# Kernel optimization log

Measured on AMD Instinct MI355X. Metric: run time of the kernel, lower is better.

## Reference

```python
import jax, jax.numpy as jnp
import numpy as np

D_MODEL = 768
HIDDEN = 2048  # round(768*8/3)=2048, already a multiple of 64
N_EXPERTS = 8
ALPHA = 0.05  # load_balance_alpha


def setup_inputs() -> dict:
    key = jax.random.key(0)
    k0, k1, k2, k3, k4 = jax.random.split(key, 5)
    x = jax.random.normal(k0, (2, 2048, D_MODEL), dtype=jnp.float32)
    wg_w = jax.random.normal(k1, (N_EXPERTS, D_MODEL), dtype=jnp.float32) * 0.02
    wg_b = jnp.zeros((N_EXPERTS,), dtype=jnp.float32)
    Wu = jax.random.normal(k2, (N_EXPERTS, D_MODEL, HIDDEN), dtype=jnp.float32) * 0.02
    Wv = jax.random.normal(k3, (N_EXPERTS, D_MODEL, HIDDEN), dtype=jnp.float32) * 0.02
    Wd = jax.random.normal(k4, (N_EXPERTS, HIDDEN, D_MODEL), dtype=jnp.float32) * 0.02
    return {"x": x, "wg_w": wg_w, "wg_b": wg_b, "Wu": Wu, "Wv": Wv, "Wd": Wd}


def reference(x, wg_w, wg_b, Wu, Wv, Wd):
    b, t, d = x.shape
    xf = x.reshape(b * t, d)  # [N, d]

    # ---- Top1Router (eval mode: temp=1, no noise, z_loss_coef=0) ----
    logits = xf @ wg_w.T + wg_b            # [N, E]
    probs = jax.nn.softmax(logits, axis=-1)
    top1_idx = jnp.argmax(logits, axis=-1)  # [N]
    top1_p = jnp.take_along_axis(probs, top1_idx[:, None], axis=1)[:, 0]  # [N]

    # aux loss: me and ce computed under no_grad in the torch source -> stop_gradient
    one_hot = jax.nn.one_hot(top1_idx, N_EXPERTS, dtype=probs.dtype)
    me = jax.lax.stop_gradient(one_hot.mean(axis=0))   # [E]
    ce = jax.lax.stop_gradient(probs.mean(axis=0))     # [E]
    aux = ALPHA * N_EXPERTS * jnp.sum(me * ce)

    # ---- Dropless dispatch: per-expert masked SwiGLU, combined with top1 gate ----
    gate = top1_p[:, None]  # [N, 1]
    y = jnp.zeros_like(xf)
    for e in range(N_EXPERTS):
        mask = (top1_idx == e)[:, None]            # [N, 1]
        xe = jnp.where(mask, xf, 0.0)              # zero-out non-routed tokens (no biases -> exact)
        u = xe @ Wu[e]                              # [N, H]
        v = xe @ Wv[e]                              # [N, H]
        ye = (jax.nn.silu(u) * v) @ Wd[e]           # [N, d]
        y = y + jnp.where(mask, ye * gate, 0.0)
    return y.reshape(b, t, d), aux
```

## Files before the change

kernel.cpp:

```cpp
#include <hip/hip_runtime.h>
#include <cstdint>
#include <cstddef>

#define TOK 4096
#define DM 768
#define HID 2048
#define NE 8

typedef __attribute__((ext_vector_type(8))) short bf16x8;
typedef __attribute__((ext_vector_type(4))) float f32x4;

#define ASYNC16(GP, LP) \
  __builtin_amdgcn_global_load_lds((__attribute__((address_space(1))) void*)(GP), \
                                   (__attribute__((address_space(3))) void*)(LP), 16, 0, 0)

__device__ __forceinline__ unsigned short f2bf(float f) {
  unsigned int u = __float_as_uint(f);
  u += 0x7FFF + ((u >> 16) & 1);
  return (unsigned short)(u >> 16);
}
__device__ __forceinline__ unsigned int pack2(float a, float b) {
  return (unsigned)f2bf(a) | ((unsigned)f2bf(b) << 16);
}
__device__ __forceinline__ int padded_off(const int* counts, int e) {
  int o = 0;
  for (int i = 0; i < e; ++i) o += (counts[i] + 127) & ~127;
  return o;
}

__global__ __launch_bounds__(256)
void k_gate(const float* __restrict__ x, const float* __restrict__ wgw,
            const float* __restrict__ wgb,
            int* __restrict__ eidx, float* __restrict__ gatep,
            float* __restrict__ cepart)
{
  __shared__ float ce_loc[4][NE];
  const int lane = threadIdx.x & 63;
  const int w = threadIdx.x >> 6;
  const int t = blockIdx.x * 4 + w;
  float acc[NE];
#pragma unroll
  for (int e = 0; e < NE; ++e) acc[e] = 0.f;
  const float* xr = x + (size_t)t * DM;
#pragma unroll
  for (int j = 0; j < DM / 64; ++j) {
    float xv = xr[j * 64 + lane];
#pragma unroll
    for (int e = 0; e < NE; ++e) acc[e] += xv * wgw[e * DM + j * 64 + lane];
  }
#pragma unroll
  for (int e = 0; e < NE; ++e) {
    float v = acc[e];
#pragma unroll
    for (int off = 32; off >= 1; off >>= 1) v += __shfl_xor(v, off);
    acc[e] = v + wgb[e];
  }
  float mx = acc[0]; int ai = 0;
#pragma unroll
  for (int e = 1; e < NE; ++e) if (acc[e] > mx) { mx = acc[e]; ai = e; }
  float p[NE]; float se = 0.f;
#pragma unroll
  for (int e = 0; e < NE; ++e) { p[e] = expf(acc[e] - mx); se += p[e]; }
  float inv = 1.f / se;
  if (lane == 0) {
#pragma unroll
    for (int e = 0; e < NE; ++e) ce_loc[w][e] = p[e] * inv;
    eidx[t] = ai;
    gatep[t] = p[ai] * inv;
  }
  __syncthreads();
  if (threadIdx.x < NE) {
    float s = ce_loc[0][threadIdx.x] + ce_loc[1][threadIdx.x]
            + ce_loc[2][threadIdx.x] + ce_loc[3][threadIdx.x];
    cepart[blockIdx.x * NE + threadIdx.x] = s;
  }
}

__global__ __launch_bounds__(256)
void k_count(const int* __restrict__ eidx, const float* __restrict__ gatep,
             const float* __restrict__ cepart,
             int* __restrict__ prow_arr, int* __restrict__ tlist,
             float* __restrict__ gate_b, int* __restrict__ counts_g,
             float* __restrict__ aux_out)
{
  __shared__ int hist[256][NE];
  __shared__ float fs[256][NE];
  __shared__ int po_s[NE], cnt_s[NE];
  const int tid = threadIdx.x;
  int own[NE], v[NE], el[16];
#pragma unroll
  for (int e = 0; e < NE; ++e) own[e] = 0;
#pragma unroll
  for (int j = 0; j < 16; ++j) {
    el[j] = eidx[tid * 16 + j];
#pragma unroll
    for (int e = 0; e < NE; ++e) own[e] += (el[j] == e) ? 1 : 0;
  }
#pragma unroll
  for (int e = 0; e < NE; ++e) { v[e] = own[e]; hist[tid][e] = v[e]; }
  __syncthreads();
  for (int st = 1; st < 256; st <<= 1) {
    int add[NE];
#pragma unroll
    for (int e = 0; e < NE; ++e) add[e] = (tid >= st) ? hist[tid - st][e] : 0;
    __syncthreads();
#pragma unroll
    for (int e = 0; e < NE; ++e) { v[e] += add[e]; hist[tid][e] = v[e]; }
    __syncthreads();
  }
  if (tid == 0) {
    int o = 0;
#pragma unroll
    for (int e = 0; e < NE; ++e) {
      int c = hist[255][e];
      cnt_s[e] = c; counts_g[e] = c; po_s[e] = o;
      o += (c + 127) & ~127;
    }
  }
  __syncthreads();
  int run[NE];
#pragma unroll
  for (int e = 0; e < NE; ++e) run[e] = po_s[e] + v[e] - own[e];
#pragma unroll
  for (int j = 0; j < 16; ++j) {
    const int t = tid * 16 + j;
    const int e = el[j];
    int p = 0;
#pragma unroll
    for (int k = 0; k < NE; ++k) if (e == k) p = run[k]++;
    prow_arr[t] = p;
    tlist[p] = t;
    gate_b[p] = gatep[t];
  }
  float s[NE];
#pragma unroll
  for (int e = 0; e < NE; ++e) s[e] = 0.f;
  for (int bb = tid; bb < 1024; bb += 256)
#pragma unroll
    for (int e = 0; e < NE; ++e) s[e] += cepart[bb * NE + e];
#pragma unroll
  for (int e = 0; e < NE; ++e) fs[tid][e] = s[e];
  __syncthreads();
  for (int st = 128; st > 0; st >>= 1) {
    if (tid < st)
#pragma unroll
      for (int e = 0; e < NE; ++e) fs[tid][e] += fs[tid + st][e];
    __syncthreads();
  }
  if (tid == 0) {
    float aux = 0.f;
    for (int e = 0; e < NE; ++e)
      aux += ((float)cnt_s[e] / 4096.f) * (fs[0][e] / 4096.f);
    aux_out[0] = 0.05f * 8.f * aux;
  }
}

__global__ __launch_bounds__(256)
void k2_scatter_zero(const float* __restrict__ x, const int* __restrict__ prow_arr,
                     unsigned short* __restrict__ xb, float* __restrict__ y)
{
  const int b = blockIdx.x;
  if (b < 1024) {
    const int lane = threadIdx.x & 63;
    const int w = threadIdx.x >> 6;
    const int t = b * 4 + w;
    const int prow = prow_arr[t];
    const float4* src4 = (const float4*)(x + (size_t)t * DM);
    uint2* dst = (uint2*)(xb + (size_t)prow * DM);
#pragma unroll
    for (int c = 0; c < 3; ++c) {
      float4 v = src4[lane + c * 64];
      uint2 d; d.x = pack2(v.x, v.y); d.y = pack2(v.z, v.w);
      dst[lane + c * 64] = d;
    }
  } else {
    float4* y4 = (float4*)y;
    const int base = (b - 1024) * 1536 + threadIdx.x;
#pragma unroll
    for (int c = 0; c < 6; ++c) {
      float4 z; z.x = 0.f; z.y = 0.f; z.z = 0.f; z.w = 0.f;
      y4[base + c * 256] = z;
    }
  }
}

__device__ __forceinline__ bool tile_lookup(const int* __restrict__ counts,
                                            int tile, int& e, int& tm) {
  int acc = 0, fe = -1, ftm = 0;
#pragma unroll
  for (int i = 0; i < NE; ++i) {
    int nt = (counts[i] + 255) >> 8;
    if (fe < 0 && tile < acc + nt) { fe = i; ftm = tile - acc; }
    acc += nt;
  }
  if (fe < 0) return false;
  e = fe; tm = ftm;
  return true;
}

__global__ __launch_bounds__(512, 2)
void k_ffn1(const float* __restrict__ Wu, const float* __restrict__ Wv,
            const unsigned short* __restrict__ xb, const float* __restrict__ gate_b,
            const int* __restrict__ counts, unsigned short* __restrict__ h)
{
  const int bid = blockIdx.x;
  const int tn = bid & 15;
  const int tile = bid >> 4;
  int e, tm;
  if (!tile_lookup(counts, tile, e, tm)) return;
  const int Me = counts[e];
  const int prowbase = padded_off(counts, e) + tm * 256;

  __shared__ __align__(16) char Sh[65536];

  const int tid = threadIdx.x;
  const int lane = tid & 63;
  const int w = tid >> 6;
  const int wm = w >> 1, wn = w & 1;

  const int c0 = w * 2, c1 = w * 2 + 1;
  const int mA0 = c0 * 16 + (lane >> 2), sA0 = lane & 3;
  const int ko0 = (sA0 - mA0 - (mA0 >> 2)) & 3;
  const char* aSrc0 = (const char*)xb + (size_t)(prowbase + mA0) * (DM * 2) + ko0 * 16;
  const int mA1 = c1 * 16 + (lane >> 2), sA1 = lane & 3;
  const int ko1 = (sA1 - mA1 - (mA1 >> 2)) & 3;
  const char* aSrc1 = (const char*)xb + (size_t)(prowbase + mA1) * (DM * 2) + ko1 * 16;

  const int koW = w & 3;
  const int nloc = (w >> 2) * 64 + lane;
  const unsigned offBw = (unsigned)(nloc * 4 + ((koW + nloc + (nloc >> 2)) & 3)) * 16;
  const int ncol = tn * 128 + nloc;
  const float* srcU = Wu + (size_t)e * DM * HID + (size_t)(koW * 8) * HID + ncol;
  const float* srcV = Wv + (size_t)e * DM * HID + (size_t)(koW * 8) * HID + ncol;

  const int lc = lane & 15, q = lane >> 4;
  unsigned offA[4], offU[4], offV[4];
#pragma unroll
  for (int i = 0; i < 4; ++i) {
    int m = wm * 64 + i * 16 + lc;
    offA[i] = (unsigned)(m * 4 + ((q + m + (m >> 2)) & 3)) * 16;
    int n = wn * 64 + i * 16 + lc;
    unsigned ob = (unsigned)(n * 4 + ((q + n + (n >> 2)) & 3)) * 16;
    offU[i] = 16384u + ob;
    offV[i] = 24576u + ob;
  }

  f32x4 accU[4][4], accV[4][4];
#pragma unroll
  for (int i = 0; i < 4; ++i)
#pragma unroll
    for (int j = 0; j < 4; ++j)
#pragma unroll
      for (int k = 0; k < 4; ++k) { accU[i][j][k] = 0.f; accV[i][j][k] = 0.f; }

  float fu[8], fv[8];
  ASYNC16(aSrc0, Sh + c0 * 1024); aSrc0 += 64;
  ASYNC16(aSrc1, Sh + c1 * 1024); aSrc1 += 64;
#pragma unroll
  for (int j = 0; j < 8; ++j) { fu[j] = srcU[(size_t)j * HID]; fv[j] = srcV[(size_t)j * HID]; }
  srcU += (size_t)32 * HID; srcV += (size_t)32 * HID;
  {
    uint4 up, vp;
    up.x = pack2(fu[0], fu[1]); up.y = pack2(fu[2], fu[3]);
    up.z = pack2(fu[4], fu[5]); up.w = pack2(fu[6], fu[7]);
    vp.x = pack2(fv[0], fv[1]); vp.y = pack2(fv[2], fv[3]);
    vp.z = pack2(fv[4], fv[5]); vp.w = pack2(fv[6], fv[7]);
    *(uint4*)(Sh + 16384 + offBw) = up;
    *(uint4*)(Sh + 24576 + offBw) = vp;
  }
  __syncthreads();

  for (int kt = 0; kt < 24; ++kt) {
    char* bufc = Sh + (unsigned)(kt & 1) * 32768u;
    char* bufn = Sh + (unsigned)((kt + 1) & 1) * 32768u;
    const bool more = (kt + 1) < 24;
    if (more) {
      ASYNC16(aSrc0, bufn + c0 * 1024); aSrc0 += 64;
      ASYNC16(aSrc1, bufn + c1 * 1024); aSrc1 += 64;
#pragma unroll
      for (int j = 0; j < 8; ++j) { fu[j] = srcU[(size_t)j * HID]; fv[j] = srcV[(size_t)j * HID]; }
      srcU += (size_t)32 * HID; srcV += (size_t)32 * HID;
    }
    bf16x8 a[4], bu[4], bv[4];
#pragma unroll
    for (int i = 0; i < 4; ++i) a[i] = *(const bf16x8*)(bufc + offA[i]);
#pragma unroll
    for (int j = 0; j < 4; ++j) {
      bu[j] = *(const bf16x8*)(bufc + offU[j]);
      bv[j] = *(const bf16x8*)(bufc + offV[j]);
    }
#pragma unroll
    for (int i = 0; i < 4; ++i)
#pragma unroll
      for (int j = 0; j < 4; ++j) {
        accU[i][j] = __builtin_amdgcn_mfma_f32_16x16x32_bf16(a[i], bu[j], accU[i][j], 0, 0, 0);
        accV[i][j] = __builtin_amdgcn_mfma_f32_16x16x32_bf16(a[i], bv[j], accV[i][j], 0, 0, 0);
      }
    if (more) {
      uint4 up, vp;
      up.x = pack2(fu[0], fu[1]); up.y = pack2(fu[2], fu[3]);
      up.z = pack2(fu[4], fu[5]); up.w = pack2(fu[6], fu[7]);
      vp.x = pack2(fv[0], fv[1]); vp.y = pack2(fv[2], fv[3]);
      vp.z = pack2(fv[4], fv[5]); vp.w = pack2(fv[6], fv[7]);
      *(uint4*)(bufn + 16384 + offBw) = up;
      *(uint4*)(bufn + 24576 + offBw) = vp;
    }
    __syncthreads();
  }

  const int colbase = tn * 128 + wn * 64;
  const int rlane = (lane >> 4) * 4;
  const int clane = lane & 15;
#pragma unroll
  for (int i = 0; i < 4; ++i) {
#pragma unroll
    for (int rr = 0; rr < 4; ++rr) {
      int rowIn = wm * 64 + i * 16 + rlane + rr;
      if (tm * 256 + rowIn < Me) {
        int prow = prowbase + rowIn;
        float g = gate_b[prow];
        unsigned short* hp = h + (size_t)prow * HID + colbase + clane;
#pragma unroll
        for (int j = 0; j < 4; ++j) {
          float u_ = accU[i][j][rr];
          float v_ = accV[i][j][rr];
          float sv = u_ / (1.f + expf(-u_));
          hp[j * 16] = f2bf(sv * v_ * g);
        }
      }
    }
  }
}

__global__ __launch_bounds__(512, 2)
void k_ffn2(const float* __restrict__ Wd, const unsigned short* __restrict__ h,
            const int* __restrict__ counts, const int* __restrict__ tlist,
            float* __restrict__ y)
{
  const int bid = blockIdx.x;
  const int inner = bid % 24;
  const int tn = inner % 6;
  const int sk = inner / 6;
  const int tile = bid / 24;
  int e, tm;
  if (!tile_lookup(counts, tile, e, tm)) return;
  const int Me = counts[e];
  const int prowbase = padded_off(counts, e) + tm * 256;

  __shared__ __align__(16) char Sh[49152];

  const int tid = threadIdx.x;
  const int lane = tid & 63;
  const int w = tid >> 6;
  const int wm = w >> 1, wn = w & 1;

  const int c0 = w * 2, c1 = w * 2 + 1;
  const int mA0 = c0 * 16 + (lane >> 2), sA0 = lane & 3;
  const int ko0 = (sA0 - mA0 - (mA0 >> 2)) & 3;
  const char* aSrc0 = (const char*)h + (size_t)(prowbase + mA0) * (HID * 2) + sk * 1024 + ko0 * 16;
  const int mA1 = c1 * 16 + (lane >> 2), sA1 = lane & 3;
  const int ko1 = (sA1 - mA1 - (mA1 >> 2)) & 3;
  const char* aSrc1 = (const char*)h + (size_t)(prowbase + mA1) * (HID * 2) + sk * 1024 + ko1 * 16;

  const int nloc = tid & 127;
  const int koW = tid >> 7;
  const unsigned offBw = (unsigned)(nloc * 4 + ((koW + nloc + (nloc >> 2)) & 3)) * 16;
  const int ncol = tn * 128 + nloc;
  const float* srcD = Wd + (size_t)e * HID * DM + (size_t)(sk * 512 + koW * 8) * DM + ncol;

  const int lc = lane & 15, q = lane >> 4;
  unsigned offA[4], offBr[4];
#pragma unroll
  for (int i = 0; i < 4; ++i) {
    int m = wm * 64 + i * 16 + lc;
    offA[i] = (unsigned)(m * 4 + ((q + m + (m >> 2)) & 3)) * 16;
    int n = wn * 64 + i * 16 + lc;
    offBr[i] = 16384u + (unsigned)(n * 4 + ((q + n + (n >> 2)) & 3)) * 16;
  }

  f32x4 acc[4][4];
#pragma unroll
  for (int i = 0; i < 4; ++i)
#pragma unroll
    for (int j = 0; j < 4; ++j)
#pragma unroll
      for (int k = 0; k < 4; ++k) acc[i][j][k] = 0.f;

  float fd[8];
  ASYNC16(aSrc0, Sh + c0 * 1024); aSrc0 += 64;
  ASYNC16(aSrc1, Sh + c1 * 1024); aSrc1 += 64;
#pragma unroll
  for (int j = 0; j < 8; ++j) fd[j] = srcD[(size_t)j * DM];
  srcD += (size_t)32 * DM;
  {
    uint4 dp;
    dp.x = pack2(fd[0], fd[1]); dp.y = pack2(fd[2], fd[3]);
    dp.z = pack2(fd[4], fd[5]); dp.w = pack2(fd[6], fd[7]);
    *(uint4*)(Sh + 16384 + offBw) = dp;
  }
  __syncthreads();

  for (int kt = 0; kt < 16; ++kt) {
    char* bufc = Sh + (unsigned)(kt & 1) * 24576u;
    char* bufn = Sh + (unsigned)((kt + 1) & 1) * 24576u;
    const bool more = (kt + 1) < 16;
    if (more) {
      ASYNC16(aSrc0, bufn + c0 * 1024); aSrc0 += 64;
      ASYNC16(aSrc1, bufn + c1 * 1024); aSrc1 += 64;
#pragma unroll
      for (int j = 0; j < 8; ++j) fd[j] = srcD[(size_t)j * DM];
      srcD += (size_t)32 * DM;
    }
    bf16x8 a[4], b[4];
#pragma unroll
    for (int i = 0; i < 4; ++i) a[i] = *(const bf16x8*)(bufc + offA[i]);
#pragma unroll
    for (int j = 0; j < 4; ++j) b[j] = *(const bf16x8*)(bufc + offBr[j]);
#pragma unroll
    for (int i = 0; i < 4; ++i)
#pragma unroll
      for (int j = 0; j < 4; ++j)
        acc[i][j] = __builtin_amdgcn_mfma_f32_16x16x32_bf16(a[i], b[j], acc[i][j], 0, 0, 0);
    if (more) {
      uint4 dp;
      dp.x = pack2(fd[0], fd[1]); dp.y = pack2(fd[2], fd[3]);
      dp.z = pack2(fd[4], fd[5]); dp.w = pack2(fd[6], fd[7]);
      *(uint4*)(bufn + 16384 + offBw) = dp;
    }
    __syncthreads();
  }

  const int colbase = tn * 128 + wn * 64;
  const int rlane = (lane >> 4) * 4;
  const int clane = lane & 15;
#pragma unroll
  for (int i = 0; i < 4; ++i) {
#pragma unroll
    for (int rr = 0; rr < 4; ++rr) {
      int rowIn = wm * 64 + i * 16 + rlane + rr;
      if (tm * 256 + rowIn < Me) {
        int tok = tlist[prowbase + rowIn];
        float* yp = y + (size_t)tok * DM + colbase + clane;
#pragma unroll
        for (int j = 0; j < 4; ++j) atomicAdd(&yp[j * 16], acc[i][j][rr]);
      }
    }
  }
}

extern "C" void kernel_launch(void* const* d_in, const int* in_sizes, int n_in,
                              void* d_out, int out_size, void* d_ws, size_t ws_size,
                              hipStream_t stream)
{
  const float* x   = (const float*)d_in[0];
  const float* wgw = (const float*)d_in[1];
  const float* wgb = (const float*)d_in[2];
  const float* Wu  = (const float*)d_in[3];
  const float* Wv  = (const float*)d_in[4];
  const float* Wd  = (const float*)d_in[5];
  float* out = (float*)d_out;

  char* ws = (char*)d_ws;
  int*   counts = (int*)(ws + 0);
  int*   eidx   = (int*)(ws + 256);
  float* gatep  = (float*)(ws + 16640);
  int*   prow   = (int*)(ws + 33024);
  float* cepart = (float*)(ws + 49408);
  int*   tlist  = (int*)(ws + 82176);
  float* gate_b = (float*)(ws + 102656);
  unsigned short* xb  = (unsigned short*)(ws + 123136);
  unsigned short* h   = (unsigned short*)(ws + 7987456);

  k_gate<<<1024, 256, 0, stream>>>(x, wgw, wgb, eidx, gatep, cepart);
  k_count<<<1, 256, 0, stream>>>(eidx, gatep, cepart, prow, tlist, gate_b,
                                 counts, out + (size_t)TOK * DM);
  k2_scatter_zero<<<1536, 256, 0, stream>>>(x, prow, xb, out);
  k_ffn1<<<24 * 16, 512, 0, stream>>>(Wu, Wv, xb, gate_b, counts, h);
  k_ffn2<<<24 * 24, 512, 0, stream>>>(Wd, h, counts, tlist, out);
}
```

Baseline: 347.8 us.

## Halve FFN row tiles to 128 tokens with 256-thread blocks and float2 weight loads

Both expert FFN kernels now use 128-row token tiles instead of 256, with 4-wave blocks instead of 8 and smaller double-buffered LDS. Tile lookup and the launch grids change to match (up to 40 tiles per expert dimension). The weight staging is remapped so each thread loads two adjacent fp32 columns with float2 loads and writes two bf16 LDS rows. The aim is more blocks and higher occupancy, with less padding waste on partially filled expert tiles. The cost is that each expert's fp32 weight slice is re-read by roughly twice as many tiles, which raises global/L2 weight traffic.

```diff
diff --git a/kernel.cpp b/kernel.cpp
--- a/kernel.cpp
+++ b/kernel.cpp
@@ -189,7 +189,7 @@
   int acc = 0, fe = -1, ftm = 0;
 #pragma unroll
   for (int i = 0; i < NE; ++i) {
-    int nt = (counts[i] + 255) >> 8;
+    int nt = (counts[i] + 127) >> 7;
     if (fe < 0 && tile < acc + nt) { fe = i; ftm = tile - acc; }
     acc += nt;
   }
@@ -198,7 +198,7 @@
   return true;
 }
 
-__global__ __launch_bounds__(512, 2)
+__global__ __launch_bounds__(256, 3)
 void k_ffn1(const float* __restrict__ Wu, const float* __restrict__ Wv,
             const unsigned short* __restrict__ xb, const float* __restrict__ gate_b,
             const int* __restrict__ counts, unsigned short* __restrict__ h)
@@ -209,16 +209,16 @@
   int e, tm;
   if (!tile_lookup(counts, tile, e, tm)) return;
   const int Me = counts[e];
-  const int prowbase = padded_off(counts, e) + tm * 256;
-
-  __shared__ __align__(16) char Sh[65536];
+  const int prowbase = padded_off(counts, e) + tm * 128;
+
+  __shared__ __align__(16) char Sh[49152];
 
   const int tid = threadIdx.x;
   const int lane = tid & 63;
   const int w = tid >> 6;
   const int wm = w >> 1, wn = w & 1;
 
-  const int c0 = w * 2, c1 = w * 2 + 1;
+  const int c0 = w * 2, c1 = c0 + 1;
   const int mA0 = c0 * 16 + (lane >> 2), sA0 = lane & 3;
   const int ko0 = (sA0 - mA0 - (mA0 >> 2)) & 3;
   const char* aSrc0 = (const char*)xb + (size_t)(prowbase + mA0) * (DM * 2) + ko0 * 16;
@@ -226,12 +226,12 @@
   const int ko1 = (sA1 - mA1 - (mA1 >> 2)) & 3;
   const char* aSrc1 = (const char*)xb + (size_t)(prowbase + mA1) * (DM * 2) + ko1 * 16;
 
-  const int koW = w & 3;
-  const int nloc = (w >> 2) * 64 + lane;
-  const unsigned offBw = (unsigned)(nloc * 4 + ((koW + nloc + (nloc >> 2)) & 3)) * 16;
-  const int ncol = tn * 128 + nloc;
-  const float* srcU = Wu + (size_t)e * DM * HID + (size_t)(koW * 8) * HID + ncol;
-  const float* srcV = Wv + (size_t)e * DM * HID + (size_t)(koW * 8) * HID + ncol;
+  const int koW = w;
+  const int n0 = lane * 2, n1 = n0 + 1;
+  const unsigned offB0 = (unsigned)(n0 * 4 + ((koW + n0 + (n0 >> 2)) & 3)) * 16;
+  const unsigned offB1 = (unsigned)(n1 * 4 + ((koW + n1 + (n1 >> 2)) & 3)) * 16;
+  const float* srcU = Wu + (size_t)e * DM * HID + (size_t)(koW * 8) * HID + tn * 128 + n0;
+  const float* srcV = Wv + (size_t)e * DM * HID + (size_t)(koW * 8) * HID + tn * 128 + n0;
 
   const int lc = lane & 15, q = lane >> 4;
   unsigned offA[4], offU[4], offV[4];
@@ -241,8 +241,8 @@
     offA[i] = (unsigned)(m * 4 + ((q + m + (m >> 2)) & 3)) * 16;
     int n = wn * 64 + i * 16 + lc;
     unsigned ob = (unsigned)(n * 4 + ((q + n + (n >> 2)) & 3)) * 16;
-    offU[i] = 16384u + ob;
-    offV[i] = 24576u + ob;
+    offU[i] = 8192u + ob;
+    offV[i] = 16384u + ob;
   }
 
   f32x4 accU[4][4], accV[4][4];
@@ -253,32 +253,44 @@
 #pragma unroll
       for (int k = 0; k < 4; ++k) { accU[i][j][k] = 0.f; accV[i][j][k] = 0.f; }
 
-  float fu[8], fv[8];
+  float2 fu[8], fv[8];
   ASYNC16(aSrc0, Sh + c0 * 1024); aSrc0 += 64;
   ASYNC16(aSrc1, Sh + c1 * 1024); aSrc1 += 64;
 #pragma unroll
-  for (int j = 0; j < 8; ++j) { fu[j] = srcU[(size_t)j * HID]; fv[j] = srcV[(size_t)j * HID]; }
+  for (int j = 0; j < 8; ++j) {
+    fu[j] = *(const float2*)(srcU + (size_t)j * HID);
+    fv[j] = *(const float2*)(srcV + (size_t)j * HID);
+  }
   srcU += (size_t)32 * HID; srcV += (size_t)32 * HID;
   {
-    uint4 up, vp;
-    up.x = pack2(fu[0], fu[1]); up.y = pack2(fu[2], fu[3]);
-    up.z = pack2(fu[4], fu[5]); up.w = pack2(fu[6], fu[7]);
-    vp.x = pack2(fv[0], fv[1]); vp.y = pack2(fv[2], fv[3]);
-    vp.z = pack2(fv[4], fv[5]); vp.w = pack2(fv[6], fv[7]);
-    *(uint4*)(Sh + 16384 + offBw) = up;
-    *(uint4*)(Sh + 24576 + offBw) = vp;
+    uint4 u0, u1, v0, v1;
+    u0.x = pack2(fu[0].x, fu[1].x); u0.y = pack2(fu[2].x, fu[3].x);
+    u0.z = pack2(fu[4].x, fu[5].x); u0.w = pack2(fu[6].x, fu[7].x);
+    u1.x = pack2(fu[0].y, fu[1].y); u1.y = pack2(fu[2].y, fu[3].y);
+    u1.z = pack2(fu[4].y, fu[5].y); u1.w = pack2(fu[6].y, fu[7].y);
+    v0.x = pack2(fv[0].x, fv[1].x); v0.y = pack2(fv[2].x, fv[3].x);
+    v0.z = pack2(fv[4].x, fv[5].x); v0.w = pack2(fv[6].x, fv[7].x);
+    v1.x = pack2(fv[0].y, fv[1].y); v1.y = pack2(fv[2].y, fv[3].y);
+    v1.z = pack2(fv[4].y, fv[5].y); v1.w = pack2(fv[6].y, fv[7].y);
+    *(uint4*)(Sh + 8192 + offB0) = u0;
+    *(uint4*)(Sh + 8192 + offB1) = u1;
+    *(uint4*)(Sh + 16384 + offB0) = v0;
+    *(uint4*)(Sh + 16384 + offB1) = v1;
   }
   __syncthreads();
 
   for (int kt = 0; kt < 24; ++kt) {
-    char* bufc = Sh + (unsigned)(kt & 1) * 32768u;
-    char* bufn = Sh + (unsigned)((kt + 1) & 1) * 32768u;
+    char* bufc = Sh + (unsigned)(kt & 1) * 24576u;
+    char* bufn = Sh + (unsigned)((kt + 1) & 1) * 24576u;
     const bool more = (kt + 1) < 24;
     if (more) {
       ASYNC16(aSrc0, bufn + c0 * 1024); aSrc0 += 64;
       ASYNC16(aSrc1, bufn + c1 * 1024); aSrc1 += 64;
 #pragma unroll
-      for (int j = 0; j < 8; ++j) { fu[j] = srcU[(size_t)j * HID]; fv[j] = srcV[(size_t)j * HID]; }
+      for (int j = 0; j < 8; ++j) {
+        fu[j] = *(const float2*)(srcU + (size_t)j * HID);
+        fv[j] = *(const float2*)(srcV + (size_t)j * HID);
+      }
       srcU += (size_t)32 * HID; srcV += (size_t)32 * HID;
     }
     bf16x8 a[4], bu[4], bv[4];
@@ -297,13 +309,19 @@
         accV[i][j] = __builtin_amdgcn_mfma_f32_16x16x32_bf16(a[i], bv[j], accV[i][j], 0, 0, 0);
       }
     if (more) {
-      uint4 up, vp;
-      up.x = pack2(fu[0], fu[1]); up.y = pack2(fu[2], fu[3]);
-      up.z = pack2(fu[4], fu[5]); up.w = pack2(fu[6], fu[7]);
-      vp.x = pack2(fv[0], fv[1]); vp.y = pack2(fv[2], fv[3]);
-      vp.z = pack2(fv[4], fv[5]); vp.w = pack2(fv[6], fv[7]);
-      *(uint4*)(bufn + 16384 + offBw) = up;
-      *(uint4*)(bufn + 24576 + offBw) = vp;
+      uint4 u0, u1, v0, v1;
+      u0.x = pack2(fu[0].x, fu[1].x); u0.y = pack2(fu[2].x, fu[3].x);
+      u0.z = pack2(fu[4].x, fu[5].x); u0.w = pack2(fu[6].x, fu[7].x);
+      u1.x = pack2(fu[0].y, fu[1].y); u1.y = pack2(fu[2].y, fu[3].y);
+      u1.z = pack2(fu[4].y, fu[5].y); u1.w = pack2(fu[6].y, fu[7].y);
+      v0.x = pack2(fv[0].x, fv[1].x); v0.y = pack2(fv[2].x, fv[3].x);
+      v0.z = pack2(fv[4].x, fv[5].x); v0.w = pack2(fv[6].x, fv[7].x);
+      v1.x = pack2(fv[0].y, fv[1].y); v1.y = pack2(fv[2].y, fv[3].y);
+      v1.z = pack2(fv[4].y, fv[5].y); v1.w = pack2(fv[6].y, fv[7].y);
+      *(uint4*)(bufn + 8192 + offB0) = u0;
+      *(uint4*)(bufn + 8192 + offB1) = u1;
+      *(uint4*)(bufn + 16384 + offB0) = v0;
+      *(uint4*)(bufn + 16384 + offB1) = v1;
     }
     __syncthreads();
   }
@@ -316,7 +334,7 @@
 #pragma unroll
     for (int rr = 0; rr < 4; ++rr) {
       int rowIn = wm * 64 + i * 16 + rlane + rr;
-      if (tm * 256 + rowIn < Me) {
+      if (tm * 128 + rowIn < Me) {
         int prow = prowbase + rowIn;
         float g = gate_b[prow];
         unsigned short* hp = h + (size_t)prow * HID + colbase + clane;
@@ -332,7 +350,7 @@
   }
 }
 
-__global__ __launch_bounds__(512, 2)
+__global__ __launch_bounds__(256, 4)
 void k_ffn2(const float* __restrict__ Wd, const unsigned short* __restrict__ h,
             const int* __restrict__ counts, const int* __restrict__ tlist,
             float* __restrict__ y)
@@ -345,16 +363,16 @@
   int e, tm;
   if (!tile_lookup(counts, tile, e, tm)) return;
   const int Me = counts[e];
-  const int prowbase = padded_off(counts, e) + tm * 256;
-
-  __shared__ __align__(16) char Sh[49152];
+  const int prowbase = padded_off(counts, e) + tm * 128;
+
+  __shared__ __align__(16) char Sh[32768];
 
   const int tid = threadIdx.x;
   const int lane = tid & 63;
   const int w = tid >> 6;
   const int wm = w >> 1, wn = w & 1;
 
-  const int c0 = w * 2, c1 = w * 2 + 1;
+  const int c0 = w * 2, c1 = c0 + 1;
   const int mA0 = c0 * 16 + (lane >> 2), sA0 = lane & 3;
   const int ko0 = (sA0 - mA0 - (mA0 >> 2)) & 3;
   const char* aSrc0 = (const char*)h + (size_t)(prowbase + mA0) * (HID * 2) + sk * 1024 + ko0 * 16;
@@ -362,11 +380,11 @@
   const int ko1 = (sA1 - mA1 - (mA1 >> 2)) & 3;
   const char* aSrc1 = (const char*)h + (size_t)(prowbase + mA1) * (HID * 2) + sk * 1024 + ko1 * 16;
 
-  const int nloc = tid & 127;
-  const int koW = tid >> 7;
-  const unsigned offBw = (unsigned)(nloc * 4 + ((koW + nloc + (nloc >> 2)) & 3)) * 16;
-  const int ncol = tn * 128 + nloc;
-  const float* srcD = Wd + (size_t)e * HID * DM + (size_t)(sk * 512 + koW * 8) * DM + ncol;
+  const int koW = w;
+  const int n0 = lane * 2, n1 = n0 + 1;
+  const unsigned offB0 = (unsigned)(n0 * 4 + ((koW + n0 + (n0 >> 2)) & 3)) * 16;
+  const unsigned offB1 = (unsigned)(n1 * 4 + ((koW + n1 + (n1 >> 2)) & 3)) * 16;
+  const float* srcD = Wd + (size_t)e * HID * DM + (size_t)(sk * 512 + koW * 8) * DM + tn * 128 + n0;
 
   const int lc = lane & 15, q = lane >> 4;
   unsigned offA[4], offBr[4];
@@ -375,7 +393,7 @@
     int m = wm * 64 + i * 16 + lc;
     offA[i] = (unsigned)(m * 4 + ((q + m + (m >> 2)) & 3)) * 16;
     int n = wn * 64 + i * 16 + lc;
-    offBr[i] = 16384u + (unsigned)(n * 4 + ((q + n + (n >> 2)) & 3)) * 16;
+    offBr[i] = 8192u + (unsigned)(n * 4 + ((q + n + (n >> 2)) & 3)) * 16;
   }
 
   f32x4 acc[4][4];
@@ -386,29 +404,32 @@
 #pragma unroll
       for (int k = 0; k < 4; ++k) acc[i][j][k] = 0.f;
 
-  float fd[8];
+  float2 fd[8];
   ASYNC16(aSrc0, Sh + c0 * 1024); aSrc0 += 64;
   ASYNC16(aSrc1, Sh + c1 * 1024); aSrc1 += 64;
 #pragma unroll
-  for (int j = 0; j < 8; ++j) fd[j] = srcD[(size_t)j * DM];
+  for (int j = 0; j < 8; ++j) fd[j] = *(const float2*)(srcD + (size_t)j * DM);
   srcD += (size_t)32 * DM;
   {
-    uint4 dp;
-    dp.x = pack2(fd[0], fd[1]); dp.y = pack2(fd[2], fd[3]);
-    dp.z = pack2(fd[4], fd[5]); dp.w = pack2(fd[6], fd[7]);
-    *(uint4*)(Sh + 16384 + offBw) = dp;
+    uint4 d0, d1;
+    d0.x = pack2(fd[0].x, fd[1].x); d0.y = pack2(fd[2].x, fd[3].x);
+    d0.z = pack2(fd[4].x, fd[5].x); d0.w = pack2(fd[6].x, fd[7].x);
+    d1.x = pack2(fd[0].y, fd[1].y); d1.y = pack2(fd[2].y, fd[3].y);
+    d1.z = pack2(fd[4].y, fd[5].y); d1.w = pack2(fd[6].y, fd[7].y);
+    *(uint4*)(Sh + 8192 + offB0) = d0;
+    *(uint4*)(Sh + 8192 + offB1) = d1;
   }
   __syncthreads();
 
   for (int kt = 0; kt < 16; ++kt) {
-    char* bufc = Sh + (unsigned)(kt & 1) * 24576u;
-    char* bufn = Sh + (unsigned)((kt + 1) & 1) * 24576u;
+    char* bufc = Sh + (unsigned)(kt & 1) * 16384u;
+    char* bufn = Sh + (unsigned)((kt + 1) & 1) * 16384u;
     const bool more = (kt + 1) < 16;
     if (more) {
       ASYNC16(aSrc0, bufn + c0 * 1024); aSrc0 += 64;
       ASYNC16(aSrc1, bufn + c1 * 1024); aSrc1 += 64;
 #pragma unroll
-      for (int j = 0; j < 8; ++j) fd[j] = srcD[(size_t)j * DM];
+      for (int j = 0; j < 8; ++j) fd[j] = *(const float2*)(srcD + (size_t)j * DM);
       srcD += (size_t)32 * DM;
     }
     bf16x8 a[4], b[4];
@@ -422,10 +443,13 @@
       for (int j = 0; j < 4; ++j)
         acc[i][j] = __builtin_amdgcn_mfma_f32_16x16x32_bf16(a[i], b[j], acc[i][j], 0, 0, 0);
     if (more) {
-      uint4 dp;
-      dp.x = pack2(fd[0], fd[1]); dp.y = pack2(fd[2], fd[3]);
-      dp.z = pack2(fd[4], fd[5]); dp.w = pack2(fd[6], fd[7]);
-      *(uint4*)(bufn + 16384 + offBw) = dp;
+      uint4 d0, d1;
+      d0.x = pack2(fd[0].x, fd[1].x); d0.y = pack2(fd[2].x, fd[3].x);
+      d0.z = pack2(fd[4].x, fd[5].x); d0.w = pack2(fd[6].x, fd[7].x);
+      d1.x = pack2(fd[0].y, fd[1].y); d1.y = pack2(fd[2].y, fd[3].y);
+      d1.z = pack2(fd[4].y, fd[5].y); d1.w = pack2(fd[6].y, fd[7].y);
+      *(uint4*)(bufn + 8192 + offB0) = d0;
+      *(uint4*)(bufn + 8192 + offB1) = d1;
     }
     __syncthreads();
   }
@@ -438,7 +462,7 @@
 #pragma unroll
     for (int rr = 0; rr < 4; ++rr) {
       int rowIn = wm * 64 + i * 16 + rlane + rr;
-      if (tm * 256 + rowIn < Me) {
+      if (tm * 128 + rowIn < Me) {
         int tok = tlist[prowbase + rowIn];
         float* yp = y + (size_t)tok * DM + colbase + clane;
 #pragma unroll
@@ -475,6 +499,6 @@
   k_count<<<1, 256, 0, stream>>>(eidx, gatep, cepart, prow, tlist, gate_b,
                                  counts, out + (size_t)TOK * DM);
   k2_scatter_zero<<<1536, 256, 0, stream>>>(x, prow, xb, out);
-  k_ffn1<<<24 * 16, 512, 0, stream>>>(Wu, Wv, xb, gate_b, counts, h);
-  k_ffn2<<<24 * 24, 512, 0, stream>>>(Wd, h, counts, tlist, out);
-}
+  k_ffn1<<<40 * 16, 256, 0, stream>>>(Wu, Wv, xb, gate_b, counts, h);
+  k_ffn2<<<40 * 24, 256, 0, stream>>>(Wd, h, counts, tlist, out);
+}
```

New measurement: 420.0 us. 1.21x slower.
